# Kernel optimization log

Measured on AMD Instinct MI355X. Metric: run time of the kernel, lower is better.

The kernel has to match this reference:

```python
import jax, jax.numpy as jnp
import numpy as np

N_USERS = 100000
EMBED_DIM = 128
N_EDGES = 640000


def setup_inputs() -> dict:
    key = jax.random.key(0)
    k1, k2, k3, k4, k5, k6 = jax.random.split(key, 6)
    # Xavier-normal-ish scale for embedding table
    emb = jax.random.normal(k1, (N_USERS, EMBED_DIM), dtype=jnp.float32) * 0.02
    s = 1.0 / np.sqrt(EMBED_DIM)
    W_l = jax.random.normal(k2, (EMBED_DIM, EMBED_DIM), dtype=jnp.float32) * s
    b_l = jax.random.normal(k3, (EMBED_DIM,), dtype=jnp.float32) * 0.01
    W_r = jax.random.normal(k4, (EMBED_DIM, EMBED_DIM), dtype=jnp.float32) * s
    src = jax.random.randint(k5, (N_EDGES,), 0, N_USERS, dtype=jnp.int64)
    dst = jax.random.randint(k6, (N_EDGES,), 0, N_USERS, dtype=jnp.int64)
    return {"emb": emb, "W_l": W_l, "b_l": b_l, "W_r": W_r, "src": src, "dst": dst}


def reference(emb, W_l, b_l, W_r, src, dst):
    # GraphSAGE (mean aggr) over the full user embedding table.
    # messages gathered from source nodes: [E, D]
    msgs = emb[src]
    agg = jax.ops.segment_sum(msgs, dst, num_segments=N_USERS)  # [N, D]
    deg = jax.ops.segment_sum(jnp.ones((dst.shape[0],), dtype=emb.dtype), dst,
                              num_segments=N_USERS)
    agg = agg / jnp.maximum(deg, 1.0)[:, None]  # mean over neighbors
    # out = lin_l(mean neighbors) + lin_r(self); bias on lin_l only (PyG SAGEConv)
    out = agg @ W_l.T + b_l + emb @ W_r.T
    # dropout (p=0) and batchnorm (is_norm=False) are identity here
    return out
```

## Files before the change

### kernel.cpp

```cpp
#include <hip/hip_runtime.h>
#include <hip/hip_bf16.h>

#define N_USERS   100000
#define EMBED_DIM 128
#define N_EDGES   640000
#define ZERO_ROW  N_USERS

typedef __bf16 bf16x8 __attribute__((ext_vector_type(8)));
typedef float  f32x4  __attribute__((ext_vector_type(4)));

#define OFF_COUNTS 25600256
#define OFF_TOTAL  26000256
#define OFF_START  26000384
#define OFF_CURSOR 26400384
#define OFF_PERM   26800384
#define OFF_WLSW   30560384
#define OFF_WRSW   30593152

__device__ __forceinline__ unsigned short f2bf_rne(float f) {
    union { float f; unsigned u; } c; c.f = f;
    unsigned u = c.u + 0x7fffu + ((c.u >> 16) & 1u);
    return (unsigned short)(u >> 16);
}
__device__ __forceinline__ float bf2f_lo(unsigned u) {
    union { float f; unsigned u; } c; c.u = u << 16;
    return c.f;
}
__device__ __forceinline__ float bf2f_hi(unsigned u) {
    union { float f; unsigned u; } c; c.u = u & 0xffff0000u;
    return c.f;
}

__global__ __launch_bounds__(256) void k_init(const float* __restrict__ emb,
                                              const float* __restrict__ Wl,
                                              const float* __restrict__ Wr,
                                              const int* __restrict__ dst,
                                              unsigned short* __restrict__ embb,
                                              int* __restrict__ counts,
                                              unsigned short* __restrict__ wlsw,
                                              unsigned short* __restrict__ wrsw) {
    int i = blockIdx.x * 256 + threadIdx.x;
    if (i < 2048) {
        int li = i & 63;
        int kt = (i >> 6) & 3;
        int jt = i >> 8;
        int row  = jt * 16 + (li & 15);
        int colb = kt * 32 + ((li >> 4) << 3);
        const float4* pl = (const float4*)(Wl + row * 128 + colb);
        const float4* pr = (const float4*)(Wr + row * 128 + colb);
        float4 l0 = pl[0], l1 = pl[1];
        float4 r0 = pr[0], r1 = pr[1];
        int o = i * 8;
        wlsw[o+0] = f2bf_rne(l0.x); wlsw[o+1] = f2bf_rne(l0.y);
        wlsw[o+2] = f2bf_rne(l0.z); wlsw[o+3] = f2bf_rne(l0.w);
        wlsw[o+4] = f2bf_rne(l1.x); wlsw[o+5] = f2bf_rne(l1.y);
        wlsw[o+6] = f2bf_rne(l1.z); wlsw[o+7] = f2bf_rne(l1.w);
        wrsw[o+0] = f2bf_rne(r0.x); wrsw[o+1] = f2bf_rne(r0.y);
        wrsw[o+2] = f2bf_rne(r0.z); wrsw[o+3] = f2bf_rne(r0.w);
        wrsw[o+4] = f2bf_rne(r1.x); wrsw[o+5] = f2bf_rne(r1.y);
        wrsw[o+6] = f2bf_rne(r1.z); wrsw[o+7] = f2bf_rne(r1.w);
    }
    if (i < 16) {
        int4 z = {0, 0, 0, 0};
        ((int4*)(embb + (size_t)ZERO_ROW * EMBED_DIM))[i] = z;
    }
    float4 a = ((const float4*)emb)[i * 2 + 0];
    float4 b = ((const float4*)emb)[i * 2 + 1];
    int4 p;
    p.x = (int)f2bf_rne(a.x) | ((int)f2bf_rne(a.y) << 16);
    p.y = (int)f2bf_rne(a.z) | ((int)f2bf_rne(a.w) << 16);
    p.z = (int)f2bf_rne(b.x) | ((int)f2bf_rne(b.y) << 16);
    p.w = (int)f2bf_rne(b.z) | ((int)f2bf_rne(b.w) << 16);
    ((int4*)embb)[i] = p;
    if (i < N_EDGES) atomicAdd(&counts[dst[i]], 1);
}

__global__ __launch_bounds__(256) void k_alloc(const int* __restrict__ counts,
                                               int* __restrict__ start,
                                               int* __restrict__ cursor,
                                               int* __restrict__ total,
                                               int* __restrict__ perm) {
    int i    = blockIdx.x * 256 + threadIdx.x;
    int lane = threadIdx.x & 63;
    int wv   = threadIdx.x >> 6;
    int4 c4 = {0, 0, 0, 0};
    if (i < 25000) c4 = ((const int4*)counts)[i];
    int4 p4;
    p4.x = (c4.x + 3) & ~3;
    p4.y = (c4.y + 3) & ~3;
    p4.z = (c4.z + 3) & ~3;
    p4.w = (c4.w + 3) & ~3;
    int csum = p4.x + p4.y + p4.z + p4.w;
    int pre = csum;
#pragma unroll
    for (int d = 1; d < 64; d <<= 1) {
        int v = __shfl_up(pre, d);
        if (lane >= d) pre += v;
    }
    __shared__ int swv[4];
    __shared__ int sgbase;
    if (lane == 63) swv[wv] = pre;
    __syncthreads();
    if (threadIdx.x == 0)
        sgbase = atomicAdd(total, swv[0] + swv[1] + swv[2] + swv[3]);
    __syncthreads();
    int waveoff = 0;
    for (int w = 0; w < wv; w++) waveoff += swv[w];
    int base = sgbase + waveoff + (pre - csum);
    if (i < 25000) {
        int4 s;
        s.x = base;
        s.y = s.x + p4.x;
        s.z = s.y + p4.y;
        s.w = s.z + p4.z;
        ((int4*)start)[i]  = s;
        ((int4*)cursor)[i] = s;
        for (int k = c4.x; k < p4.x; k++) perm[s.x + k] = ZERO_ROW;
        for (int k = c4.y; k < p4.y; k++) perm[s.y + k] = ZERO_ROW;
        for (int k = c4.z; k < p4.z; k++) perm[s.z + k] = ZERO_ROW;
        for (int k = c4.w; k < p4.w; k++) perm[s.w + k] = ZERO_ROW;
    }
}

__global__ __launch_bounds__(256) void k_perm(const int* __restrict__ src,
                                              const int* __restrict__ dst,
                                              int* __restrict__ cursor,
                                              int* __restrict__ perm) {
    int e = blockIdx.x * 256 + threadIdx.x;
    if (e < N_EDGES) {
        int pos = atomicAdd(&cursor[dst[e]], 1);
        perm[pos] = src[e];
    }
}

#define LDS_S 136
__global__ __launch_bounds__(256, 4) void k_fused(const unsigned short* __restrict__ embb,
                                                  const int* __restrict__ start,
                                                  const int* __restrict__ counts,
                                                  const int* __restrict__ perm,
                                                  const unsigned short* __restrict__ wlsw,
                                                  const unsigned short* __restrict__ wrsw,
                                                  const float* __restrict__ bl,
                                                  float* __restrict__ out) {
    __shared__ unsigned short sa[32 * LDS_S];
    __shared__ unsigned short se[32 * LDS_S];
    int tid  = threadIdx.x;
    int wave = tid >> 6;
    int lane = tid & 63;
    int quad = lane >> 4;
    int m    = lane & 15;
    int node0 = blockIdx.x * 32;

    const int4* eslab = (const int4*)(embb + (size_t)node0 * EMBED_DIM);
    int4 ve0 = eslab[tid];
    int4 ve1 = eslab[256 + tid];

    const unsigned short* ep = embb;
    int off = lane * 2;
#pragma unroll
    for (int p = 0; p < 4; p++) {
        int nA = node0 + wave * 8 + p * 2;
        int nB = nA + 1;
        int sA = start[nA], cntA = counts[nA];
        int sB = start[nB], cntB = counts[nB];
        int ga = (cntA + 3) >> 2;
        int gb = (cntB + 3) >> 2;
        int gmin = ga < gb ? ga : gb;
        float2 accA = {0.f, 0.f}, accB = {0.f, 0.f};
        int t = 0;
#pragma unroll 2
        for (; t < gmin; t++) {
            int4 ia = ((const int4*)(perm + sA))[t];
            int4 ib = ((const int4*)(perm + sB))[t];
            unsigned a0 = *(const unsigned*)(ep + (size_t)ia.x * EMBED_DIM + off);
            unsigned a1 = *(const unsigned*)(ep + (size_t)ia.y * EMBED_DIM + off);
            unsigned a2 = *(const unsigned*)(ep + (size_t)ia.z * EMBED_DIM + off);
            unsigned a3 = *(const unsigned*)(ep + (size_t)ia.w * EMBED_DIM + off);
            unsigned b0 = *(const unsigned*)(ep + (size_t)ib.x * EMBED_DIM + off);
            unsigned b1 = *(const unsigned*)(ep + (size_t)ib.y * EMBED_DIM + off);
            unsigned b2 = *(const unsigned*)(ep + (size_t)ib.z * EMBED_DIM + off);
            unsigned b3 = *(const unsigned*)(ep + (size_t)ib.w * EMBED_DIM + off);
            accA.x += (bf2f_lo(a0) + bf2f_lo(a1)) + (bf2f_lo(a2) + bf2f_lo(a3));
            accA.y += (bf2f_hi(a0) + bf2f_hi(a1)) + (bf2f_hi(a2) + bf2f_hi(a3));
            accB.x += (bf2f_lo(b0) + bf2f_lo(b1)) + (bf2f_lo(b2) + bf2f_lo(b3));
            accB.y += (bf2f_hi(b0) + bf2f_hi(b1)) + (bf2f_hi(b2) + bf2f_hi(b3));
        }
        for (int ta = t; ta < ga; ta++) {
            int4 ia = ((const int4*)(perm + sA))[ta];
            unsigned a0 = *(const unsigned*)(ep + (size_t)ia.x * EMBED_DIM + off);
            unsigned a1 = *(const unsigned*)(ep + (size_t)ia.y * EMBED_DIM + off);
            unsigned a2 = *(const unsigned*)(ep + (size_t)ia.z * EMBED_DIM + off);
            unsigned a3 = *(const unsigned*)(ep + (size_t)ia.w * EMBED_DIM + off);
            accA.x += (bf2f_lo(a0) + bf2f_lo(a1)) + (bf2f_lo(a2) + bf2f_lo(a3));
            accA.y += (bf2f_hi(a0) + bf2f_hi(a1)) + (bf2f_hi(a2) + bf2f_hi(a3));
        }
        for (int tb = t; tb < gb; tb++) {
            int4 ib = ((const int4*)(perm + sB))[tb];
            unsigned b0 = *(const unsigned*)(ep + (size_t)ib.x * EMBED_DIM + off);
            unsigned b1 = *(const unsigned*)(ep + (size_t)ib.y * EMBED_DIM + off);
            unsigned b2 = *(const unsigned*)(ep + (size_t)ib.z * EMBED_DIM + off);
            unsigned b3 = *(const unsigned*)(ep + (size_t)ib.w * EMBED_DIM + off);
            accB.x += (bf2f_lo(b0) + bf2f_lo(b1)) + (bf2f_lo(b2) + bf2f_lo(b3));
            accB.y += (bf2f_hi(b0) + bf2f_hi(b1)) + (bf2f_hi(b2) + bf2f_hi(b3));
        }
        float invA = (cntA > 0) ? 1.0f / (float)cntA : 0.0f;
        float invB = (cntB > 0) ? 1.0f / (float)cntB : 0.0f;
        unsigned oA = (unsigned)f2bf_rne(accA.x * invA) | ((unsigned)f2bf_rne(accA.y * invA) << 16);
        unsigned oB = (unsigned)f2bf_rne(accB.x * invB) | ((unsigned)f2bf_rne(accB.y * invB) << 16);
        int nlA = wave * 8 + p * 2;
        *(unsigned*)(sa + nlA * LDS_S + off)       = oA;
        *(unsigned*)(sa + (nlA + 1) * LDS_S + off) = oB;
    }

    {
        int g = tid, row = g >> 4, c = g & 15;
        *(int4*)(se + row * LDS_S + c * 8) = ve0;
        g = 256 + tid; row = g >> 4; c = g & 15;
        *(int4*)(se + row * LDS_S + c * 8) = ve1;
    }

    int jt0 = wave * 2;
    bf16x8 wl[2][4], wr[2][4];
#pragma unroll
    for (int jj = 0; jj < 2; jj++) {
#pragma unroll
        for (int kt = 0; kt < 4; kt++) {
            size_t o = (size_t)((((jt0 + jj) * 4 + kt) * 64 + lane)) * 8;
            wl[jj][kt] = *(const bf16x8*)((const __bf16*)wlsw + o);
            wr[jj][kt] = *(const bf16x8*)((const __bf16*)wrsw + o);
        }
    }
    float bias[2];
    bias[0] = bl[(jt0 + 0) * 16 + m];
    bias[1] = bl[(jt0 + 1) * 16 + m];

    __syncthreads();

#pragma unroll
    for (int rt = 0; rt < 2; rt++) {
        bf16x8 af[4], ef[4];
#pragma unroll
        for (int kt = 0; kt < 4; kt++) {
            int o = (rt * 16 + m) * LDS_S + kt * 32 + quad * 8;
            af[kt] = *(const bf16x8*)(sa + o);
            ef[kt] = *(const bf16x8*)(se + o);
        }
        f32x4 acc[2] = {{0.f,0.f,0.f,0.f}, {0.f,0.f,0.f,0.f}};
#pragma unroll
        for (int kt = 0; kt < 4; kt++) {
#pragma unroll
            for (int jj = 0; jj < 2; jj++) {
                acc[jj] = __builtin_amdgcn_mfma_f32_16x16x32_bf16(af[kt], wl[jj][kt], acc[jj], 0, 0, 0);
                acc[jj] = __builtin_amdgcn_mfma_f32_16x16x32_bf16(ef[kt], wr[jj][kt], acc[jj], 0, 0, 0);
            }
        }
#pragma unroll
        for (int jj = 0; jj < 2; jj++) {
#pragma unroll
            for (int r = 0; r < 4; r++) {
                int orow = node0 + rt * 16 + quad * 4 + r;
                out[(size_t)orow * EMBED_DIM + (jt0 + jj) * 16 + m] = acc[jj][r] + bias[jj];
            }
        }
    }
}

extern "C" void kernel_launch(void* const* d_in, const int* in_sizes, int n_in,
                              void* d_out, int out_size, void* d_ws, size_t ws_size,
                              hipStream_t stream) {
    const float* emb = (const float*)d_in[0];
    const float* Wl  = (const float*)d_in[1];
    const float* bl  = (const float*)d_in[2];
    const float* Wr  = (const float*)d_in[3];
    const int*   src = (const int*)d_in[4];
    const int*   dst = (const int*)d_in[5];
    float* out = (float*)d_out;

    char* ws = (char*)d_ws;
    unsigned short* embb   = (unsigned short*)ws;
    int*            counts = (int*)(ws + OFF_COUNTS);
    int*            total  = (int*)(ws + OFF_TOTAL);
    int*            start  = (int*)(ws + OFF_START);
    int*            cursor = (int*)(ws + OFF_CURSOR);
    int*            perm   = (int*)(ws + OFF_PERM);
    unsigned short* wlsw   = (unsigned short*)(ws + OFF_WLSW);
    unsigned short* wrsw   = (unsigned short*)(ws + OFF_WRSW);

    hipMemsetAsync(ws + OFF_COUNTS, 0, (OFF_TOTAL - OFF_COUNTS) + 4, stream);

    k_init<<<6250, 256, 0, stream>>>(emb, Wl, Wr, dst, embb, counts, wlsw, wrsw);
    k_alloc<<<98, 256, 0, stream>>>(counts, start, cursor, total, perm);
    k_perm<<<2500, 256, 0, stream>>>(src, dst, cursor, perm);
    k_fused<<<3125, 256, 0, stream>>>(embb, start, counts, perm, wlsw, wrsw, bl, out);
}
```

Baseline: 214.3 us.

## Balance neighbor aggregation across waves using flat edge groups and LDS atomics

Result: slower. 317.9 us (+48.3%).

```diff
diff --git a/kernel.cpp b/kernel.cpp
--- a/kernel.cpp
+++ b/kernel.cpp
@@ -5,8 +5,11 @@
 #define EMBED_DIM 128
 #define N_EDGES   640000
 #define ZERO_ROW  N_USERS
+#define LOC_SHIFT 20
+#define ID_MASK   0xFFFFF
 
 typedef __bf16 bf16x8 __attribute__((ext_vector_type(8)));
+typedef unsigned short u16x8 __attribute__((ext_vector_type(8)));
 typedef float  f32x4  __attribute__((ext_vector_type(4)));
 
 #define OFF_COUNTS 25600256
@@ -115,10 +118,15 @@
         s.w = s.z + p4.z;
         ((int4*)start)[i]  = s;
         ((int4*)cursor)[i] = s;
-        for (int k = c4.x; k < p4.x; k++) perm[s.x + k] = ZERO_ROW;
-        for (int k = c4.y; k < p4.y; k++) perm[s.y + k] = ZERO_ROW;
-        for (int k = c4.z; k < p4.z; k++) perm[s.z + k] = ZERO_ROW;
-        for (int k = c4.w; k < p4.w; k++) perm[s.w + k] = ZERO_ROW;
+        int n0 = i * 4;
+        int zx = ZERO_ROW | (((n0 + 0) & 31) << LOC_SHIFT);
+        int zy = ZERO_ROW | (((n0 + 1) & 31) << LOC_SHIFT);
+        int zz = ZERO_ROW | (((n0 + 2) & 31) << LOC_SHIFT);
+        int zw = ZERO_ROW | (((n0 + 3) & 31) << LOC_SHIFT);
+        for (int k = c4.x; k < p4.x; k++) perm[s.x + k] = zx;
+        for (int k = c4.y; k < p4.y; k++) perm[s.y + k] = zy;
+        for (int k = c4.z; k < p4.z; k++) perm[s.z + k] = zz;
+        for (int k = c4.w; k < p4.w; k++) perm[s.w + k] = zw;
     }
 }
 
@@ -128,13 +136,15 @@
                                               int* __restrict__ perm) {
     int e = blockIdx.x * 256 + threadIdx.x;
     if (e < N_EDGES) {
-        int pos = atomicAdd(&cursor[dst[e]], 1);
-        perm[pos] = src[e];
-    }
-}
-
-#define LDS_S 136
-__global__ __launch_bounds__(256, 4) void k_fused(const unsigned short* __restrict__ embb,
+        int d = dst[e];
+        int pos = atomicAdd(&cursor[d], 1);
+        perm[pos] = src[e] | ((d & 31) << LOC_SHIFT);
+    }
+}
+
+#define LDS_S  136
+#define SACC_S 132
+__global__ __launch_bounds__(256, 6) void k_fused(const unsigned short* __restrict__ embb,
                                                   const int* __restrict__ start,
                                                   const int* __restrict__ counts,
                                                   const int* __restrict__ perm,
@@ -142,7 +152,7 @@
                                                   const unsigned short* __restrict__ wrsw,
                                                   const float* __restrict__ bl,
                                                   float* __restrict__ out) {
-    __shared__ unsigned short sa[32 * LDS_S];
+    __shared__ float          s_acc[32 * SACC_S];
     __shared__ unsigned short se[32 * LDS_S];
     int tid  = threadIdx.x;
     int wave = tid >> 6;
@@ -150,66 +160,36 @@
     int quad = lane >> 4;
     int m    = lane & 15;
     int node0 = blockIdx.x * 32;
+    int off   = lane * 2;
 
     const int4* eslab = (const int4*)(embb + (size_t)node0 * EMBED_DIM);
     int4 ve0 = eslab[tid];
     int4 ve1 = eslab[256 + tid];
 
+    int cR0 = counts[node0 + m];
+    int cR1 = counts[node0 + 16 + m];
+
+    for (int z = tid; z < 32 * SACC_S; z += 256) s_acc[z] = 0.0f;
+    __syncthreads();
+
+    int gbase = start[node0];
+    int nL    = node0 + 31;
+    int gend  = start[nL] + ((counts[nL] + 3) & ~3);
+    int ngroups = (gend - gbase) >> 2;
+    const int4* gp = (const int4*)(perm + gbase);
     const unsigned short* ep = embb;
-    int off = lane * 2;
-#pragma unroll
-    for (int p = 0; p < 4; p++) {
-        int nA = node0 + wave * 8 + p * 2;
-        int nB = nA + 1;
-        int sA = start[nA], cntA = counts[nA];
-        int sB = start[nB], cntB = counts[nB];
-        int ga = (cntA + 3) >> 2;
-        int gb = (cntB + 3) >> 2;
-        int gmin = ga < gb ? ga : gb;
-        float2 accA = {0.f, 0.f}, accB = {0.f, 0.f};
-        int t = 0;
 #pragma unroll 2
-        for (; t < gmin; t++) {
-            int4 ia = ((const int4*)(perm + sA))[t];
-            int4 ib = ((const int4*)(perm + sB))[t];
-            unsigned a0 = *(const unsigned*)(ep + (size_t)ia.x * EMBED_DIM + off);
-            unsigned a1 = *(const unsigned*)(ep + (size_t)ia.y * EMBED_DIM + off);
-            unsigned a2 = *(const unsigned*)(ep + (size_t)ia.z * EMBED_DIM + off);
-            unsigned a3 = *(const unsigned*)(ep + (size_t)ia.w * EMBED_DIM + off);
-            unsigned b0 = *(const unsigned*)(ep + (size_t)ib.x * EMBED_DIM + off);
-            unsigned b1 = *(const unsigned*)(ep + (size_t)ib.y * EMBED_DIM + off);
-            unsigned b2 = *(const unsigned*)(ep + (size_t)ib.z * EMBED_DIM + off);
-            unsigned b3 = *(const unsigned*)(ep + (size_t)ib.w * EMBED_DIM + off);
-            accA.x += (bf2f_lo(a0) + bf2f_lo(a1)) + (bf2f_lo(a2) + bf2f_lo(a3));
-            accA.y += (bf2f_hi(a0) + bf2f_hi(a1)) + (bf2f_hi(a2) + bf2f_hi(a3));
-            accB.x += (bf2f_lo(b0) + bf2f_lo(b1)) + (bf2f_lo(b2) + bf2f_lo(b3));
-            accB.y += (bf2f_hi(b0) + bf2f_hi(b1)) + (bf2f_hi(b2) + bf2f_hi(b3));
-        }
-        for (int ta = t; ta < ga; ta++) {
-            int4 ia = ((const int4*)(perm + sA))[ta];
-            unsigned a0 = *(const unsigned*)(ep + (size_t)ia.x * EMBED_DIM + off);
-            unsigned a1 = *(const unsigned*)(ep + (size_t)ia.y * EMBED_DIM + off);
-            unsigned a2 = *(const unsigned*)(ep + (size_t)ia.z * EMBED_DIM + off);
-            unsigned a3 = *(const unsigned*)(ep + (size_t)ia.w * EMBED_DIM + off);
-            accA.x += (bf2f_lo(a0) + bf2f_lo(a1)) + (bf2f_lo(a2) + bf2f_lo(a3));
-            accA.y += (bf2f_hi(a0) + bf2f_hi(a1)) + (bf2f_hi(a2) + bf2f_hi(a3));
-        }
-        for (int tb = t; tb < gb; tb++) {
-            int4 ib = ((const int4*)(perm + sB))[tb];
-            unsigned b0 = *(const unsigned*)(ep + (size_t)ib.x * EMBED_DIM + off);
-            unsigned b1 = *(const unsigned*)(ep + (size_t)ib.y * EMBED_DIM + off);
-            unsigned b2 = *(const unsigned*)(ep + (size_t)ib.z * EMBED_DIM + off);
-            unsigned b3 = *(const unsigned*)(ep + (size_t)ib.w * EMBED_DIM + off);
-            accB.x += (bf2f_lo(b0) + bf2f_lo(b1)) + (bf2f_lo(b2) + bf2f_lo(b3));
-            accB.y += (bf2f_hi(b0) + bf2f_hi(b1)) + (bf2f_hi(b2) + bf2f_hi(b3));
-        }
-        float invA = (cntA > 0) ? 1.0f / (float)cntA : 0.0f;
-        float invB = (cntB > 0) ? 1.0f / (float)cntB : 0.0f;
-        unsigned oA = (unsigned)f2bf_rne(accA.x * invA) | ((unsigned)f2bf_rne(accA.y * invA) << 16);
-        unsigned oB = (unsigned)f2bf_rne(accB.x * invB) | ((unsigned)f2bf_rne(accB.y * invB) << 16);
-        int nlA = wave * 8 + p * 2;
-        *(unsigned*)(sa + nlA * LDS_S + off)       = oA;
-        *(unsigned*)(sa + (nlA + 1) * LDS_S + off) = oB;
+    for (int g = wave; g < ngroups; g += 4) {
+        int4 q4 = gp[g];
+        int loc = (q4.x >> LOC_SHIFT) & 31;
+        unsigned a0 = *(const unsigned*)(ep + (size_t)(q4.x & ID_MASK) * EMBED_DIM + off);
+        unsigned a1 = *(const unsigned*)(ep + (size_t)(q4.y & ID_MASK) * EMBED_DIM + off);
+        unsigned a2 = *(const unsigned*)(ep + (size_t)(q4.z & ID_MASK) * EMBED_DIM + off);
+        unsigned a3 = *(const unsigned*)(ep + (size_t)(q4.w & ID_MASK) * EMBED_DIM + off);
+        float lo = (bf2f_lo(a0) + bf2f_lo(a1)) + (bf2f_lo(a2) + bf2f_lo(a3));
+        float hi = (bf2f_hi(a0) + bf2f_hi(a1)) + (bf2f_hi(a2) + bf2f_hi(a3));
+        atomicAdd(&s_acc[loc * SACC_S + off],     lo);
+        atomicAdd(&s_acc[loc * SACC_S + off + 1], hi);
     }
 
     {
@@ -233,16 +213,28 @@
     float bias[2];
     bias[0] = bl[(jt0 + 0) * 16 + m];
     bias[1] = bl[(jt0 + 1) * 16 + m];
+    float inv[2];
+    inv[0] = (cR0 > 0) ? 1.0f / (float)cR0 : 0.0f;
+    inv[1] = (cR1 > 0) ? 1.0f / (float)cR1 : 0.0f;
 
     __syncthreads();
 
 #pragma unroll
     for (int rt = 0; rt < 2; rt++) {
+        float iv = inv[rt];
         bf16x8 af[4], ef[4];
 #pragma unroll
         for (int kt = 0; kt < 4; kt++) {
+            const float* pr = s_acc + (rt * 16 + m) * SACC_S + kt * 32 + quad * 8;
+            f32x4 x0 = *(const f32x4*)pr;
+            f32x4 x1 = *(const f32x4*)(pr + 4);
+            u16x8 ua;
+            ua[0] = f2bf_rne(x0[0] * iv); ua[1] = f2bf_rne(x0[1] * iv);
+            ua[2] = f2bf_rne(x0[2] * iv); ua[3] = f2bf_rne(x0[3] * iv);
+            ua[4] = f2bf_rne(x1[0] * iv); ua[5] = f2bf_rne(x1[1] * iv);
+            ua[6] = f2bf_rne(x1[2] * iv); ua[7] = f2bf_rne(x1[3] * iv);
+            af[kt] = *(bf16x8*)&ua;
             int o = (rt * 16 + m) * LDS_S + kt * 32 + quad * 8;
-            af[kt] = *(const bf16x8*)(sa + o);
             ef[kt] = *(const bf16x8*)(se + o);
         }
         f32x4 acc[2] = {{0.f,0.f,0.f,0.f}, {0.f,0.f,0.f,0.f}};
```

## Split wave into half-waves gathering 8-byte rows and drop self-embedding LDS staging

Applied to the files above, without the earlier changes.

Measured after the change: 220.6 us. 2.9% more time.

```diff
diff --git a/kernel.cpp b/kernel.cpp
--- a/kernel.cpp
+++ b/kernel.cpp
@@ -134,89 +134,101 @@
 }
 
 #define LDS_S 136
-__global__ __launch_bounds__(256, 4) void k_fused(const unsigned short* __restrict__ embb,
-                                                  const int* __restrict__ start,
-                                                  const int* __restrict__ counts,
-                                                  const int* __restrict__ perm,
-                                                  const unsigned short* __restrict__ wlsw,
-                                                  const unsigned short* __restrict__ wrsw,
-                                                  const float* __restrict__ bl,
-                                                  float* __restrict__ out) {
+__global__ __launch_bounds__(256) void k_fused(const unsigned short* __restrict__ embb,
+                                               const int* __restrict__ start,
+                                               const int* __restrict__ counts,
+                                               const int* __restrict__ perm,
+                                               const unsigned short* __restrict__ wlsw,
+                                               const unsigned short* __restrict__ wrsw,
+                                               const float* __restrict__ bl,
+                                               float* __restrict__ out) {
     __shared__ unsigned short sa[32 * LDS_S];
-    __shared__ unsigned short se[32 * LDS_S];
     int tid  = threadIdx.x;
     int wave = tid >> 6;
     int lane = tid & 63;
     int quad = lane >> 4;
     int m    = lane & 15;
+    int half = lane >> 5;
+    int colb = (lane & 31) * 4;
     int node0 = blockIdx.x * 32;
 
-    const int4* eslab = (const int4*)(embb + (size_t)node0 * EMBED_DIM);
-    int4 ve0 = eslab[tid];
-    int4 ve1 = eslab[256 + tid];
+    int nb = node0 + wave * 8;
+    int sN[8], cN[8];
+#pragma unroll
+    for (int r = 0; r < 8; r++) { sN[r] = start[nb + r]; cN[r] = counts[nb + r]; }
 
     const unsigned short* ep = embb;
-    int off = lane * 2;
+
 #pragma unroll
     for (int p = 0; p < 4; p++) {
-        int nA = node0 + wave * 8 + p * 2;
-        int nB = nA + 1;
-        int sA = start[nA], cntA = counts[nA];
-        int sB = start[nB], cntB = counts[nB];
-        int ga = (cntA + 3) >> 2;
-        int gb = (cntB + 3) >> 2;
+        int nA = p * 2, nB = nA + 1;
+        const int4* gA = (const int4*)(perm + sN[nA]);
+        const int4* gB = (const int4*)(perm + sN[nB]);
+        int ga = (cN[nA] + 3) >> 2;
+        int gb = (cN[nB] + 3) >> 2;
         int gmin = ga < gb ? ga : gb;
-        float2 accA = {0.f, 0.f}, accB = {0.f, 0.f};
+        f32x4 aA = {0.f, 0.f, 0.f, 0.f}, aB = {0.f, 0.f, 0.f, 0.f};
         int t = 0;
 #pragma unroll 2
         for (; t < gmin; t++) {
-            int4 ia = ((const int4*)(perm + sA))[t];
-            int4 ib = ((const int4*)(perm + sB))[t];
-            unsigned a0 = *(const unsigned*)(ep + (size_t)ia.x * EMBED_DIM + off);
-            unsigned a1 = *(const unsigned*)(ep + (size_t)ia.y * EMBED_DIM + off);
-            unsigned a2 = *(const unsigned*)(ep + (size_t)ia.z * EMBED_DIM + off);
-            unsigned a3 = *(const unsigned*)(ep + (size_t)ia.w * EMBED_DIM + off);
-            unsigned b0 = *(const unsigned*)(ep + (size_t)ib.x * EMBED_DIM + off);
-            unsigned b1 = *(const unsigned*)(ep + (size_t)ib.y * EMBED_DIM + off);
-            unsigned b2 = *(const unsigned*)(ep + (size_t)ib.z * EMBED_DIM + off);
-            unsigned b3 = *(const unsigned*)(ep + (size_t)ib.w * EMBED_DIM + off);
-            accA.x += (bf2f_lo(a0) + bf2f_lo(a1)) + (bf2f_lo(a2) + bf2f_lo(a3));
-            accA.y += (bf2f_hi(a0) + bf2f_hi(a1)) + (bf2f_hi(a2) + bf2f_hi(a3));
-            accB.x += (bf2f_lo(b0) + bf2f_lo(b1)) + (bf2f_lo(b2) + bf2f_lo(b3));
-            accB.y += (bf2f_hi(b0) + bf2f_hi(b1)) + (bf2f_hi(b2) + bf2f_hi(b3));
+            int4 qa = gA[t];
+            int4 qb = gB[t];
+            int ra0 = half ? qa.y : qa.x;
+            int ra1 = half ? qa.w : qa.z;
+            int rb0 = half ? qb.y : qb.x;
+            int rb1 = half ? qb.w : qb.z;
+            uint2 ua0 = *(const uint2*)(ep + (size_t)ra0 * EMBED_DIM + colb);
+            uint2 ua1 = *(const uint2*)(ep + (size_t)ra1 * EMBED_DIM + colb);
+            uint2 ub0 = *(const uint2*)(ep + (size_t)rb0 * EMBED_DIM + colb);
+            uint2 ub1 = *(const uint2*)(ep + (size_t)rb1 * EMBED_DIM + colb);
+            aA[0] += bf2f_lo(ua0.x) + bf2f_lo(ua1.x);
+            aA[1] += bf2f_hi(ua0.x) + bf2f_hi(ua1.x);
+            aA[2] += bf2f_lo(ua0.y) + bf2f_lo(ua1.y);
+            aA[3] += bf2f_hi(ua0.y) + bf2f_hi(ua1.y);
+            aB[0] += bf2f_lo(ub0.x) + bf2f_lo(ub1.x);
+            aB[1] += bf2f_hi(ub0.x) + bf2f_hi(ub1.x);
+            aB[2] += bf2f_lo(ub0.y) + bf2f_lo(ub1.y);
+            aB[3] += bf2f_hi(ub0.y) + bf2f_hi(ub1.y);
         }
         for (int ta = t; ta < ga; ta++) {
-            int4 ia = ((const int4*)(perm + sA))[ta];
-            unsigned a0 = *(const unsigned*)(ep + (size_t)ia.x * EMBED_DIM + off);
-            unsigned a1 = *(const unsigned*)(ep + (size_t)ia.y * EMBED_DIM + off);
-            unsigned a2 = *(const unsigned*)(ep + (size_t)ia.z * EMBED_DIM + off);
-            unsigned a3 = *(const unsigned*)(ep + (size_t)ia.w * EMBED_DIM + off);
-            accA.x += (bf2f_lo(a0) + bf2f_lo(a1)) + (bf2f_lo(a2) + bf2f_lo(a3));
-            accA.y += (bf2f_hi(a0) + bf2f_hi(a1)) + (bf2f_hi(a2) + bf2f_hi(a3));
+            int4 qa = gA[ta];
+            int ra0 = half ? qa.y : qa.x;
+            int ra1 = half ? qa.w : qa.z;
+            uint2 ua0 = *(const uint2*)(ep + (size_t)ra0 * EMBED_DIM + colb);
+            uint2 ua1 = *(const uint2*)(ep + (size_t)ra1 * EMBED_DIM + colb);
+            aA[0] += bf2f_lo(ua0.x) + bf2f_lo(ua1.x);
+            aA[1] += bf2f_hi(ua0.x) + bf2f_hi(ua1.x);
+            aA[2] += bf2f_lo(ua0.y) + bf2f_lo(ua1.y);
+            aA[3] += bf2f_hi(ua0.y) + bf2f_hi(ua1.y);
         }
         for (int tb = t; tb < gb; tb++) {
-            int4 ib = ((const int4*)(perm + sB))[tb];
-            unsigned b0 = *(const unsigned*)(ep + (size_t)ib.x * EMBED_DIM + off);
-            unsigned b1 = *(const unsigned*)(ep + (size_t)ib.y * EMBED_DIM + off);
-            unsigned b2 = *(const unsigned*)(ep + (size_t)ib.z * EMBED_DIM + off);
-            unsigned b3 = *(const unsigned*)(ep + (size_t)ib.w * EMBED_DIM + off);
-            accB.x += (bf2f_lo(b0) + bf2f_lo(b1)) + (bf2f_lo(b2) + bf2f_lo(b3));
-            accB.y += (bf2f_hi(b0) + bf2f_hi(b1)) + (bf2f_hi(b2) + bf2f_hi(b3));
-        }
-        float invA = (cntA > 0) ? 1.0f / (float)cntA : 0.0f;
-        float invB = (cntB > 0) ? 1.0f / (float)cntB : 0.0f;
-        unsigned oA = (unsigned)f2bf_rne(accA.x * invA) | ((unsigned)f2bf_rne(accA.y * invA) << 16);
-        unsigned oB = (unsigned)f2bf_rne(accB.x * invB) | ((unsigned)f2bf_rne(accB.y * invB) << 16);
-        int nlA = wave * 8 + p * 2;
-        *(unsigned*)(sa + nlA * LDS_S + off)       = oA;
-        *(unsigned*)(sa + (nlA + 1) * LDS_S + off) = oB;
-    }
-
-    {
-        int g = tid, row = g >> 4, c = g & 15;
-        *(int4*)(se + row * LDS_S + c * 8) = ve0;
-        g = 256 + tid; row = g >> 4; c = g & 15;
-        *(int4*)(se + row * LDS_S + c * 8) = ve1;
+            int4 qb = gB[tb];
+            int rb0 = half ? qb.y : qb.x;
+            int rb1 = half ? qb.w : qb.z;
+            uint2 ub0 = *(const uint2*)(ep + (size_t)rb0 * EMBED_DIM + colb);
+            uint2 ub1 = *(const uint2*)(ep + (size_t)rb1 * EMBED_DIM + colb);
+            aB[0] += bf2f_lo(ub0.x) + bf2f_lo(ub1.x);
+            aB[1] += bf2f_hi(ub0.x) + bf2f_hi(ub1.x);
+            aB[2] += bf2f_lo(ub0.y) + bf2f_lo(ub1.y);
+            aB[3] += bf2f_hi(ub0.y) + bf2f_hi(ub1.y);
+        }
+#pragma unroll
+        for (int j = 0; j < 4; j++) {
+            aA[j] += __shfl_xor(aA[j], 32);
+            aB[j] += __shfl_xor(aB[j], 32);
+        }
+        float invA = (cN[nA] > 0) ? 1.0f / (float)cN[nA] : 0.0f;
+        float invB = (cN[nB] > 0) ? 1.0f / (float)cN[nB] : 0.0f;
+        unsigned dA0 = (unsigned)f2bf_rne(aA[0] * invA) | ((unsigned)f2bf_rne(aA[1] * invA) << 16);
+        unsigned dA1 = (unsigned)f2bf_rne(aA[2] * invA) | ((unsigned)f2bf_rne(aA[3] * invA) << 16);
+        unsigned dB0 = (unsigned)f2bf_rne(aB[0] * invB) | ((unsigned)f2bf_rne(aB[1] * invB) << 16);
+        unsigned dB1 = (unsigned)f2bf_rne(aB[2] * invB) | ((unsigned)f2bf_rne(aB[3] * invB) << 16);
+        if (lane < 32) {
+            uint2 vA; vA.x = dA0; vA.y = dA1;
+            uint2 vB; vB.x = dB0; vB.y = dB1;
+            *(uint2*)(sa + (wave * 8 + nA) * LDS_S + colb) = vA;
+            *(uint2*)(sa + (wave * 8 + nB) * LDS_S + colb) = vB;
+        }
     }
 
     int jt0 = wave * 2;
@@ -243,7 +255,8 @@
         for (int kt = 0; kt < 4; kt++) {
             int o = (rt * 16 + m) * LDS_S + kt * 32 + quad * 8;
             af[kt] = *(const bf16x8*)(sa + o);
-            ef[kt] = *(const bf16x8*)(se + o);
+            ef[kt] = *(const bf16x8*)(embb + (size_t)(node0 + rt * 16 + m) * EMBED_DIM
+                                      + kt * 32 + quad * 8);
         }
         f32x4 acc[2] = {{0.f,0.f,0.f,0.f}, {0.f,0.f,0.f,0.f}};
 #pragma unroll
```
